# Kernel tuning notes

Measured on AMD Instinct MI355X. Metric: run time of the kernel, lower is better.

The kernel has to match this reference:

```python
import jax, jax.numpy as jnp
import numpy as np

B, S, D, H, E, P, TOP_K = 8, 4096, 512, 2048, 8, 16, 2


def setup_inputs() -> dict:
    key = jax.random.key(0)
    ks = jax.random.split(key, 7)
    x = jax.random.normal(ks[0], (B, S, D), dtype=jnp.float32)
    pattern_ids = jax.random.randint(ks[1], (B,), 0, P)
    # router params (init per module: std 0.01 content, std 0.1 pattern bias)
    Wr = 0.01 * jax.random.normal(ks[2], (D, E), dtype=jnp.float32)
    Wp = 0.1 * jax.random.normal(ks[3], (P, E), dtype=jnp.float32)
    # per-expert SwiGLU FFN weights (stacked): w1, w3: [E,D,H], w2: [E,H,D]
    W1 = jax.random.normal(ks[4], (E, D, H), dtype=jnp.float32) / np.float32(np.sqrt(D))
    W2 = jax.random.normal(ks[5], (E, H, D), dtype=jnp.float32) / np.float32(np.sqrt(H))
    W3 = jax.random.normal(ks[6], (E, D, H), dtype=jnp.float32) / np.float32(np.sqrt(D))
    return {"x": x, "pattern_ids": pattern_ids, "Wr": Wr, "Wp": Wp, "W1": W1, "W2": W2, "W3": W3}


def reference(x, pattern_ids, Wr, Wp, W1, W2, W3):
    num_experts = W1.shape[0]
    num_patterns = Wp.shape[0]
    # ---- pattern-aware router ----
    # content logits + per-batch pattern bias broadcast over seq
    logits = jnp.einsum('bsd,de->bse', x, Wr) + Wp[pattern_ids][:, None, :]  # [B,S,E]
    top_w, top_i = jax.lax.top_k(logits, TOP_K)           # [B,S,K]
    gates = jax.nn.softmax(top_w, axis=-1)                # softmax over the top-k logits
    # ---- expert dispatch / combine (loop over small fixed expert count) ----
    y = jnp.zeros_like(x)
    for e in range(num_experts):
        # combined gate weight for expert e per token (0 if not selected)
        w_e = jnp.sum(gates * (top_i == e), axis=-1)      # [B,S]
        h = jnp.einsum('bsd,dh->bsh', x, W1[e]) * jax.nn.silu(jnp.einsum('bsd,dh->bsh', x, W3[e]))
        y = y + w_e[..., None] * jnp.einsum('bsh,hd->bsd', h, W2[e])
    # ---- auxiliary losses ----
    probs = jax.nn.softmax(logits, axis=-1)
    router_z_loss = jnp.mean(jnp.square(logits)) * 0.001
    balance_loss = jnp.mean(jnp.square(probs.mean(axis=(0, 1)) - 1.0 / num_experts))
    Pn = jax.nn.softmax(Wp, axis=-1)
    sim = Pn @ Pn.T
    specialization_loss = jnp.mean(sim * (1.0 - jnp.eye(num_patterns, dtype=sim.dtype))) * 0.1
    return (y, router_z_loss, balance_loss, specialization_loss)
```

## Files before the change

### kernel.cpp

```cpp
#include <hip/hip_runtime.h>
#include <hip/hip_bf16.h>
#include <math.h>


#define B_ 8
#define S_ 4096
#define D_ 512
#define H_ 2048
#define E_ 8
#define P_ 16
#define NTOK (B_ * S_)
#define NPAIR (NTOK * 2)

typedef __bf16 bf16;
typedef __bf16 bf16x8 __attribute__((ext_vector_type(8)));
typedef float f32x4 __attribute__((ext_vector_type(4)));

#define OFF_GATES 256
#define OFF_LIST (OFF_GATES + NPAIR * 4)
#define OFF_XBF (OFF_LIST + E_ * NTOK * 4)
#define OFF_W13T (OFF_XBF + (size_t)NTOK * D_ * 2)
#define OFF_W2T (OFF_W13T + (size_t)E_ * 2 * H_ * D_ * 2)
#define OFF_HBUF (OFF_W2T + (size_t)E_ * D_ * H_ * 2)
#define WS_NEEDED (OFF_HBUF + (size_t)NTOK * H_ * 2)

__device__ __forceinline__ void gl16(const bf16* g, bf16* l) {
  __builtin_amdgcn_global_load_lds((const __attribute__((address_space(1))) unsigned int*)g,
                                   (__attribute__((address_space(3))) unsigned int*)l, 16, 0, 0);
}

__global__ __launch_bounds__(256) void router_kernel(
    const float* __restrict__ x, const int* __restrict__ pids,
    const float* __restrict__ Wr, const float* __restrict__ Wp,
    bf16* __restrict__ xbf, float* __restrict__ gates, int* __restrict__ lists,
    int* __restrict__ counts, float* __restrict__ probSum, float* __restrict__ zSum) {
  __shared__ float xs[32 * 516];
  __shared__ float wr_s[E_ * 516];
  __shared__ float wp_s[E_];
  __shared__ float probAcc[E_];
  __shared__ float zAcc;
  __shared__ int lcnt[E_], lbase[E_];
  __shared__ float lg_s[32][E_ + 1];

  const int tid = threadIdx.x;
  const int tok0 = blockIdx.x * 32;

#pragma unroll
  for (int rep = 0; rep < (D_ * E_) / 256; ++rep) {
    int flat = rep * 256 + tid;
    wr_s[(flat & 7) * 516 + (flat >> 3)] = Wr[flat];
  }
  if (tid < E_) {
    wp_s[tid] = Wp[pids[tok0 >> 12] * E_ + tid];
    probAcc[tid] = 0.f;
    lcnt[tid] = 0;
  }
  if (tid == 0) zAcc = 0.f;

  const float4* x4 = (const float4*)(x + (size_t)tok0 * D_);
#pragma unroll
  for (int rep = 0; rep < 16; ++rep) {
    int idx = rep * 256 + tid;
    float4 v = x4[idx];
    int t = idx >> 7;
    int d = (idx & 127) * 4;
    *(float4*)(xs + t * 516 + d) = v;
    union { unsigned short u[4]; uint2 qq; } pk;
    pk.u[0] = __builtin_bit_cast(unsigned short, (bf16)v.x);
    pk.u[1] = __builtin_bit_cast(unsigned short, (bf16)v.y);
    pk.u[2] = __builtin_bit_cast(unsigned short, (bf16)v.z);
    pk.u[3] = __builtin_bit_cast(unsigned short, (bf16)v.w);
    *(uint2*)(xbf + (size_t)tok0 * D_ + (size_t)idx * 4) = pk.qq;
  }
  __syncthreads();

  const int t = tid >> 3, e = tid & 7;
  const int lane = tid & 63;
  {
    float a0 = 0.f, a1 = 0.f, a2 = 0.f, a3 = 0.f;
    const float* xr = xs + t * 516;
    const float* wr = wr_s + e * 516;
#pragma unroll 8
    for (int d = 0; d < D_; d += 4) {
      float4 xv = *(const float4*)(xr + d);
      float4 wv = *(const float4*)(wr + d);
      a0 += xv.x * wv.x;
      a1 += xv.y * wv.y;
      a2 += xv.z * wv.z;
      a3 += xv.w * wv.w;
    }
    lg_s[t][e] = (a0 + a1) + (a2 + a3) + wp_s[e];
  }
  __syncthreads();

  float v[E_];
#pragma unroll
  for (int k = 0; k < E_; ++k) v[k] = lg_s[t][k];
  const float lg = v[e];
  float m = v[0];
#pragma unroll
  for (int k = 1; k < E_; ++k) m = fmaxf(m, v[k]);
  float s = 0.f;
#pragma unroll
  for (int k = 0; k < E_; ++k) s += expf(v[k] - m);
  float prob = expf(lg - m) / s;
  float z = lg * lg;
  int i1 = 0;
  float v1 = v[0];
#pragma unroll
  for (int k = 1; k < E_; ++k)
    if (v[k] > v1) { v1 = v[k]; i1 = k; }
  int i2 = -1;
  float v2 = -1e30f;
#pragma unroll
  for (int k = 0; k < E_; ++k)
    if (k != i1 && v[k] > v2) { v2 = v[k]; i2 = k; }

  float p = prob;
  p += __shfl_xor(p, 8);
  p += __shfl_xor(p, 16);
  p += __shfl_xor(p, 32);
  float zz = z;
#pragma unroll
  for (int off = 1; off < 64; off <<= 1) zz += __shfl_xor(zz, off);
  if (lane < 8) atomicAdd(&probAcc[e], p);
  if (lane == 0) atomicAdd(&zAcc, zz);

  int r = (e == i1) ? 0 : ((e == i2) ? 1 : -1);
  int pos = -1;
  if (r >= 0) {
    float ex = expf(v2 - v1);
    float g = (r == 0) ? 1.f / (1.f + ex) : ex / (1.f + ex);
    gates[(tok0 + t) * 2 + r] = g;
    pos = atomicAdd(&lcnt[e], 1);
  }
  __syncthreads();
  if (tid < E_) lbase[tid] = atomicAdd(&counts[tid], lcnt[tid]);
  __syncthreads();
  if (r >= 0) lists[e * NTOK + lbase[e] + pos] = (tok0 + t) * 2 + r;
  if (tid < E_) atomicAdd(&probSum[tid], probAcc[tid]);
  else if (tid == 8) atomicAdd(zSum, zAcc);
}

__global__ __launch_bounds__(256) void transpose_convert(const float* __restrict__ in,
                                                         bf16* __restrict__ out, int R, int C,
                                                         size_t out_estride, int mode) {
  const int e = blockIdx.z;
  const int r0 = blockIdx.y * 64, c0 = blockIdx.x * 64;
  in += (size_t)e * R * C;
  out += (size_t)e * out_estride;
  __shared__ unsigned int lt[64 * 33];

  const int tid = threadIdx.x;
  const int m = tid & 15, qq = tid >> 4;
#pragma unroll
  for (int rep = 0; rep < 2; ++rep) {
    int rp = qq + rep * 16;
    const float4 a = *(const float4*)(in + (size_t)(r0 + rp * 2) * C + c0 + m * 4);
    const float4 b = *(const float4*)(in + (size_t)(r0 + rp * 2 + 1) * C + c0 + m * 4);
#pragma unroll
    for (int j = 0; j < 4; ++j) {
      unsigned short lo = __builtin_bit_cast(unsigned short, (bf16)((&a.x)[j]));
      unsigned short hi = __builtin_bit_cast(unsigned short, (bf16)((&b.x)[j]));
      lt[(m * 4 + j) * 33 + rp] = (unsigned int)lo | ((unsigned int)hi << 16);
    }
  }
  __syncthreads();
  const int c = tid >> 2, dw0 = (tid & 3) * 8;
  unsigned int vv[8];
#pragma unroll
  for (int j = 0; j < 8; ++j) vv[j] = lt[c * 33 + dw0 + j];
  int orow = c0 + c;
  if (mode >= 0) orow = ((orow >> 4) << 5) | (orow & 15) | mode;
  uint4* dst = (uint4*)(out + (size_t)orow * R + r0 + dw0 * 2);
  dst[0] = make_uint4(vv[0], vv[1], vv[2], vv[3]);
  dst[1] = make_uint4(vv[4], vv[5], vv[6], vv[7]);
}

__global__ __launch_bounds__(256, 2) void gemm1_kernel(
    const bf16* __restrict__ xbf, const bf16* __restrict__ W13T,
    const int* __restrict__ counts, const int* __restrict__ lists,
    const float* __restrict__ gates, bf16* __restrict__ hbuf, int e) {
  const int count = counts[e];
  const int m0 = blockIdx.y * 128;
  if (m0 >= count) return;
  const int n0 = blockIdx.x * 128;
  const int* list_e = lists + e * NTOK;
  const bf16* Be = W13T + (size_t)e * (2 * H_) * D_;

  __shared__ bf16 sA[4 * 128 * 32];
  __shared__ bf16 sB[4 * 128 * 32];
  __shared__ int stok[128];
  __shared__ float sgate[128];

  const int tid = threadIdx.x;
  if (tid < 128) {
    int rg = m0 + tid;
    int pr = (rg < count) ? list_e[rg] : 0;
    stok[tid] = pr >> 1;
    sgate[tid] = (rg < count) ? gates[pr] : 0.f;
  }
  __syncthreads();

  const int wave = tid >> 6, lane = tid & 63;
  const int rsub = lane >> 2, kq = lane & 3;
  const int scol = (kq ^ ((lane >> 3) & 3)) * 8;
  const int rA0 = wave * 16 + rsub, rA1 = 64 + wave * 16 + rsub;
  const bf16* aP0 = xbf + (size_t)stok[rA0] * D_ + scol;
  const bf16* aP1 = xbf + (size_t)stok[rA1] * D_ + scol;
  const bf16* bP0 = Be + (size_t)(n0 + rA0) * D_ + scol;
  const bf16* bP1 = Be + (size_t)(n0 + rA1) * D_ + scol;

  const int wm = wave >> 1, wn = wave & 1;
  const int lm = lane & 15, q = lane >> 4;
  const int rq = (q ^ ((lm >> 1) & 3)) * 8;
  const bf16* aRd = sA + (wm * 64 + lm) * 32 + rq;
  const bf16* bRd = sB + (wn * 64 + lm) * 32 + rq;

  f32x4 acc[4][4] = {};

  auto STAGE = [&](int t, int bi) {
    const int ko = t * 32;
    bf16* ba = sA + bi * 4096;
    bf16* bb = sB + bi * 4096;
    gl16(aP0 + ko, ba + wave * 512);
    gl16(aP1 + ko, ba + (wave + 4) * 512);
    gl16(bP0 + ko, bb + wave * 512);
    gl16(bP1 + ko, bb + (wave + 4) * 512);
  };
  auto COMP = [&](int bi) {
    const bf16* aR = aRd + bi * 4096;
    const bf16* bR = bRd + bi * 4096;
    bf16x8 af[4], bf_[4];
#pragma unroll
    for (int i = 0; i < 4; ++i) {
      af[i] = *(const bf16x8*)(aR + i * 512);
      bf_[i] = *(const bf16x8*)(bR + i * 512);
    }
#pragma unroll
    for (int mt = 0; mt < 4; ++mt)
#pragma unroll
      for (int nt = 0; nt < 4; ++nt)
        acc[mt][nt] =
            __builtin_amdgcn_mfma_f32_16x16x32_bf16(af[mt], bf_[nt], acc[mt][nt], 0, 0, 0);
  };

  STAGE(0, 0);
  STAGE(1, 1);
  for (int t = 0; t < D_ / 32 - 2; ++t) {
    STAGE(t + 2, (t + 2) & 3);
    asm volatile("s_waitcnt vmcnt(8) lgkmcnt(0)" ::: "memory");
    __builtin_amdgcn_s_barrier();
    COMP(t & 3);
  }
  asm volatile("s_waitcnt vmcnt(4) lgkmcnt(0)" ::: "memory");
  __builtin_amdgcn_s_barrier();
  COMP((D_ / 32 - 2) & 3);
  asm volatile("s_waitcnt vmcnt(0) lgkmcnt(0)" ::: "memory");
  __builtin_amdgcn_s_barrier();
  COMP((D_ / 32 - 1) & 3);

  const int hb = (n0 >> 1) + wn * 32;
#pragma unroll
  for (int mt = 0; mt < 4; ++mt) {
#pragma unroll
    for (int u = 0; u < 2; ++u) {
#pragma unroll
      for (int r = 0; r < 4; ++r) {
        int lrow = wm * 64 + mt * 16 + q * 4 + r;
        int grow = m0 + lrow;
        if (grow < count) {
          float v1 = acc[mt][2 * u][r];
          float v3 = acc[mt][2 * u + 1][r];
          float g = v1 * (v3 / (1.f + __expf(-v3))) * sgate[lrow];
          hbuf[(size_t)grow * H_ + hb + u * 16 + lm] = (bf16)g;
        }
      }
    }
  }
}

__global__ __launch_bounds__(256, 2) void gemm2_kernel(const bf16* __restrict__ hbuf,
                                                       const bf16* __restrict__ W2T,
                                                       const int* __restrict__ counts,
                                                       const int* __restrict__ lists,
                                                       float* __restrict__ y, int e) {
  const int count = counts[e];
  const int m0 = blockIdx.y * 128;
  if (m0 >= count) return;
  const int n0 = blockIdx.x * 128;
  const int kb = blockIdx.z * (H_ / 2);
  const bf16* W2e = W2T + (size_t)e * D_ * H_;
  const int* list_e = lists + e * NTOK;

  __shared__ bf16 sA[4 * 128 * 32];
  __shared__ bf16 sB[4 * 128 * 32];
  __shared__ int stok[128];

  const int tid = threadIdx.x;
  if (tid < 128) {
    int rg = m0 + tid;
    stok[tid] = (rg < count) ? (list_e[rg] >> 1) : 0;
  }
  __syncthreads();

  const int wave = tid >> 6, lane = tid & 63;
  const int rsub = lane >> 2, kq = lane & 3;
  const int scol = (kq ^ ((lane >> 3) & 3)) * 8;
  const int rA0 = wave * 16 + rsub, rA1 = 64 + wave * 16 + rsub;
  const bf16* aP0 = hbuf + (size_t)(m0 + rA0) * H_ + kb + scol;
  const bf16* aP1 = hbuf + (size_t)(m0 + rA1) * H_ + kb + scol;
  const bf16* bP0 = W2e + (size_t)(n0 + rA0) * H_ + kb + scol;
  const bf16* bP1 = W2e + (size_t)(n0 + rA1) * H_ + kb + scol;

  const int wm = wave >> 1, wn = wave & 1;
  const int lm = lane & 15, q = lane >> 4;
  const int rq = (q ^ ((lm >> 1) & 3)) * 8;
  const bf16* aRd = sA + (wm * 64 + lm) * 32 + rq;
  const bf16* bRd = sB + (wn * 64 + lm) * 32 + rq;

  f32x4 acc[4][4] = {};

  auto STAGE = [&](int t, int bi) {
    const int ko = t * 32;
    bf16* ba = sA + bi * 4096;
    bf16* bb = sB + bi * 4096;
    gl16(aP0 + ko, ba + wave * 512);
    gl16(aP1 + ko, ba + (wave + 4) * 512);
    gl16(bP0 + ko, bb + wave * 512);
    gl16(bP1 + ko, bb + (wave + 4) * 512);
  };
  auto COMP = [&](int bi) {
    const bf16* aR = aRd + bi * 4096;
    const bf16* bR = bRd + bi * 4096;
    bf16x8 af[4], bf_[4];
#pragma unroll
    for (int i = 0; i < 4; ++i) {
      af[i] = *(const bf16x8*)(aR + i * 512);
      bf_[i] = *(const bf16x8*)(bR + i * 512);
    }
#pragma unroll
    for (int mt = 0; mt < 4; ++mt)
#pragma unroll
      for (int nt = 0; nt < 4; ++nt)
        acc[mt][nt] =
            __builtin_amdgcn_mfma_f32_16x16x32_bf16(af[mt], bf_[nt], acc[mt][nt], 0, 0, 0);
  };

  const int NT = (H_ / 2) / 32;
  STAGE(0, 0);
  STAGE(1, 1);
  for (int t = 0; t < NT - 2; ++t) {
    STAGE(t + 2, (t + 2) & 3);
    asm volatile("s_waitcnt vmcnt(8) lgkmcnt(0)" ::: "memory");
    __builtin_amdgcn_s_barrier();
    COMP(t & 3);
  }
  asm volatile("s_waitcnt vmcnt(4) lgkmcnt(0)" ::: "memory");
  __builtin_amdgcn_s_barrier();
  COMP((NT - 2) & 3);
  asm volatile("s_waitcnt vmcnt(0) lgkmcnt(0)" ::: "memory");
  __builtin_amdgcn_s_barrier();
  COMP((NT - 1) & 3);

#pragma unroll
  for (int mt = 0; mt < 4; ++mt) {
#pragma unroll
    for (int nt = 0; nt < 4; ++nt) {
#pragma unroll
      for (int r = 0; r < 4; ++r) {
        int lrow = wm * 64 + mt * 16 + q * 4 + r;
        int grow = m0 + lrow;
        if (grow < count) {
          atomicAdd(&y[(size_t)stok[lrow] * D_ + n0 + wn * 64 + nt * 16 + lm], acc[mt][nt][r]);
        }
      }
    }
  }
}

__global__ __launch_bounds__(256) void finalize_kernel(const float* __restrict__ Wp,
                                                       const float* __restrict__ probSum,
                                                       const float* __restrict__ zSum,
                                                       float* __restrict__ out) {
  __shared__ float pn[P_][E_];
  __shared__ float simAcc;
  const int tid = threadIdx.x;
  if (tid == 0) simAcc = 0.f;
  if (tid < P_) {
    float v[E_], m = -1e30f, s = 0.f;
#pragma unroll
    for (int e = 0; e < E_; ++e) {
      v[e] = Wp[tid * E_ + e];
      m = fmaxf(m, v[e]);
    }
#pragma unroll
    for (int e = 0; e < E_; ++e) {
      float ex = expf(v[e] - m);
      pn[tid][e] = ex;
      s += ex;
    }
#pragma unroll
    for (int e = 0; e < E_; ++e) pn[tid][e] /= s;
  }
  __syncthreads();
  {
    int i = tid >> 4, j = tid & 15;
    if (i != j) {
      float d = 0.f;
#pragma unroll
      for (int e = 0; e < E_; ++e) d += pn[i][e] * pn[j][e];
      atomicAdd(&simAcc, d);
    }
  }
  __syncthreads();
  if (tid == 0) {
    out[0] = zSum[0] / (float)(NTOK * E_) * 0.001f;
    float bl = 0.f;
#pragma unroll
    for (int e = 0; e < E_; ++e) {
      float pm = probSum[e] / (float)NTOK - 1.f / (float)E_;
      bl += pm * pm;
    }
    out[1] = bl / (float)E_;
    out[2] = simAcc / (float)(P_ * P_) * 0.1f;
  }
}

extern "C" void kernel_launch(void* const* d_in, const int* in_sizes, int n_in, void* d_out,
                              int out_size, void* d_ws, size_t ws_size, hipStream_t stream) {
  const float* x = (const float*)d_in[0];
  const int* pids = (const int*)d_in[1];
  const float* Wr = (const float*)d_in[2];
  const float* Wp = (const float*)d_in[3];
  const float* W1 = (const float*)d_in[4];
  const float* W2 = (const float*)d_in[5];
  const float* W3 = (const float*)d_in[6];
  float* y = (float*)d_out;

  if (ws_size < WS_NEEDED) return;

  char* ws = (char*)d_ws;
  int* counts = (int*)ws;
  float* probSum = (float*)(ws + 32);
  float* zSum = (float*)(ws + 64);
  float* gates = (float*)(ws + OFF_GATES);
  int* lists = (int*)(ws + OFF_LIST);
  bf16* xbf = (bf16*)(ws + OFF_XBF);
  bf16* W13T = (bf16*)(ws + OFF_W13T);
  bf16* W2T = (bf16*)(ws + OFF_W2T);
  bf16* hbuf = (bf16*)(ws + OFF_HBUF);

  hipMemsetAsync(ws, 0, 256, stream);
  hipMemsetAsync(d_out, 0, (size_t)NTOK * D_ * 4, stream);

  router_kernel<<<dim3(NTOK / 32), 256, 0, stream>>>(x, pids, Wr, Wp, xbf, gates, lists, counts,
                                                     probSum, zSum);
  transpose_convert<<<dim3(H_ / 64, D_ / 64, E_), 256, 0, stream>>>(W1, W13T, D_, H_,
                                                                    (size_t)2 * H_ * D_, 0);
  transpose_convert<<<dim3(H_ / 64, D_ / 64, E_), 256, 0, stream>>>(W3, W13T, D_, H_,
                                                                    (size_t)2 * H_ * D_, 16);
  transpose_convert<<<dim3(D_ / 64, H_ / 64, E_), 256, 0, stream>>>(W2, W2T, H_, D_,
                                                                    (size_t)H_ * D_, -1);

  for (int e = 0; e < E_; ++e) {
    gemm1_kernel<<<dim3((2 * H_) / 128, NTOK / 128), 256, 0, stream>>>(xbf, W13T, counts, lists,
                                                                       gates, hbuf, e);
    gemm2_kernel<<<dim3(D_ / 128, NTOK / 128, 2), 256, 0, stream>>>(hbuf, W2T, counts, lists, y,
                                                                    e);
  }
  finalize_kernel<<<1, 256, 0, stream>>>(Wp, probSum, zSum, y + (size_t)NTOK * D_);
}
```

Before: 1.111 ms.

## Load A operand directly into registers, bypassing LDS in expert GEMMs

Both expert GEMM kernels stop staging the activation (A) tile through shared memory. Each wave instead loads its MFMA A fragments directly from global memory into double-buffered registers, while B stays in the LDS pipeline. This removes A's LDS writes and reads and halves LDS usage. In exchange, A is fetched twice, once per N-wave, through the cache, and load latency depends on register prefetch depth.

```diff
diff --git a/kernel.cpp b/kernel.cpp
--- a/kernel.cpp
+++ b/kernel.cpp
@@ -28,6 +28,17 @@
   __builtin_amdgcn_global_load_lds((const __attribute__((address_space(1))) unsigned int*)g,
                                    (__attribute__((address_space(3))) unsigned int*)l, 16, 0, 0);
 }
+
+#define WAITV(n)                                                      \
+  do {                                                                \
+    asm volatile("s_waitcnt vmcnt(" #n ") lgkmcnt(0)" ::: "memory");  \
+    __builtin_amdgcn_sched_barrier(0);                                \
+  } while (0)
+#define BARR()                                                        \
+  do {                                                                \
+    __builtin_amdgcn_s_barrier();                                     \
+    __builtin_amdgcn_sched_barrier(0);                                \
+  } while (0)
 
 __global__ __launch_bounds__(256) void router_kernel(
     const float* __restrict__ x, const int* __restrict__ pids,
@@ -188,7 +199,6 @@
   const int* list_e = lists + e * NTOK;
   const bf16* Be = W13T + (size_t)e * (2 * H_) * D_;
 
-  __shared__ bf16 sA[4 * 128 * 32];
   __shared__ bf16 sB[4 * 128 * 32];
   __shared__ int stok[128];
   __shared__ float sgate[128];
@@ -206,37 +216,35 @@
   const int rsub = lane >> 2, kq = lane & 3;
   const int scol = (kq ^ ((lane >> 3) & 3)) * 8;
   const int rA0 = wave * 16 + rsub, rA1 = 64 + wave * 16 + rsub;
-  const bf16* aP0 = xbf + (size_t)stok[rA0] * D_ + scol;
-  const bf16* aP1 = xbf + (size_t)stok[rA1] * D_ + scol;
   const bf16* bP0 = Be + (size_t)(n0 + rA0) * D_ + scol;
   const bf16* bP1 = Be + (size_t)(n0 + rA1) * D_ + scol;
 
   const int wm = wave >> 1, wn = wave & 1;
   const int lm = lane & 15, q = lane >> 4;
   const int rq = (q ^ ((lm >> 1) & 3)) * 8;
-  const bf16* aRd = sA + (wm * 64 + lm) * 32 + rq;
   const bf16* bRd = sB + (wn * 64 + lm) * 32 + rq;
 
+  const bf16* aPtr[4];
+#pragma unroll
+  for (int mt = 0; mt < 4; ++mt)
+    aPtr[mt] = xbf + (size_t)stok[wm * 64 + mt * 16 + lm] * D_ + q * 8;
+
   f32x4 acc[4][4] = {};
 
   auto STAGE = [&](int t, int bi) {
-    const int ko = t * 32;
-    bf16* ba = sA + bi * 4096;
     bf16* bb = sB + bi * 4096;
-    gl16(aP0 + ko, ba + wave * 512);
-    gl16(aP1 + ko, ba + (wave + 4) * 512);
-    gl16(bP0 + ko, bb + wave * 512);
-    gl16(bP1 + ko, bb + (wave + 4) * 512);
-  };
-  auto COMP = [&](int bi) {
-    const bf16* aR = aRd + bi * 4096;
+    gl16(bP0 + t * 32, bb + wave * 512);
+    gl16(bP1 + t * 32, bb + (wave + 4) * 512);
+  };
+  auto LOADA = [&](bf16x8 (&dst)[4], int t) {
+#pragma unroll
+    for (int mt = 0; mt < 4; ++mt) dst[mt] = *(const bf16x8*)(aPtr[mt] + t * 32);
+  };
+  auto COMP = [&](int bi, const bf16x8 (&af)[4]) {
     const bf16* bR = bRd + bi * 4096;
-    bf16x8 af[4], bf_[4];
-#pragma unroll
-    for (int i = 0; i < 4; ++i) {
-      af[i] = *(const bf16x8*)(aR + i * 512);
-      bf_[i] = *(const bf16x8*)(bR + i * 512);
-    }
+    bf16x8 bf_[4];
+#pragma unroll
+    for (int i = 0; i < 4; ++i) bf_[i] = *(const bf16x8*)(bR + i * 512);
 #pragma unroll
     for (int mt = 0; mt < 4; ++mt)
 #pragma unroll
@@ -245,20 +253,31 @@
             __builtin_amdgcn_mfma_f32_16x16x32_bf16(af[mt], bf_[nt], acc[mt][nt], 0, 0, 0);
   };
 
+  const int NT = D_ / 32;
+  bf16x8 aE[4], aO[4];
   STAGE(0, 0);
   STAGE(1, 1);
-  for (int t = 0; t < D_ / 32 - 2; ++t) {
+  LOADA(aE, 0);
+  LOADA(aO, 1);
+  for (int tt = 0; tt < (NT - 2) / 2; ++tt) {
+    const int t = 2 * tt;
     STAGE(t + 2, (t + 2) & 3);
-    asm volatile("s_waitcnt vmcnt(8) lgkmcnt(0)" ::: "memory");
-    __builtin_amdgcn_s_barrier();
-    COMP(t & 3);
-  }
-  asm volatile("s_waitcnt vmcnt(4) lgkmcnt(0)" ::: "memory");
-  __builtin_amdgcn_s_barrier();
-  COMP((D_ / 32 - 2) & 3);
-  asm volatile("s_waitcnt vmcnt(0) lgkmcnt(0)" ::: "memory");
-  __builtin_amdgcn_s_barrier();
-  COMP((D_ / 32 - 1) & 3);
+    WAITV(6);
+    BARR();
+    COMP(t & 3, aE);
+    LOADA(aE, t + 2);
+    STAGE(t + 3, (t + 3) & 3);
+    WAITV(6);
+    BARR();
+    COMP((t + 1) & 3, aO);
+    LOADA(aO, t + 3);
+  }
+  WAITV(4);
+  BARR();
+  COMP((NT - 2) & 3, aE);
+  WAITV(0);
+  BARR();
+  COMP((NT - 1) & 3, aO);
 
   const int hb = (n0 >> 1) + wn * 32;
 #pragma unroll
@@ -293,7 +312,6 @@
   const bf16* W2e = W2T + (size_t)e * D_ * H_;
   const int* list_e = lists + e * NTOK;
 
-  __shared__ bf16 sA[4 * 128 * 32];
   __shared__ bf16 sB[4 * 128 * 32];
   __shared__ int stok[128];
 
@@ -308,37 +326,35 @@
   const int rsub = lane >> 2, kq = lane & 3;
   const int scol = (kq ^ ((lane >> 3) & 3)) * 8;
   const int rA0 = wave * 16 + rsub, rA1 = 64 + wave * 16 + rsub;
-  const bf16* aP0 = hbuf + (size_t)(m0 + rA0) * H_ + kb + scol;
-  const bf16* aP1 = hbuf + (size_t)(m0 + rA1) * H_ + kb + scol;
   const bf16* bP0 = W2e + (size_t)(n0 + rA0) * H_ + kb + scol;
   const bf16* bP1 = W2e + (size_t)(n0 + rA1) * H_ + kb + scol;
 
   const int wm = wave >> 1, wn = wave & 1;
   const int lm = lane & 15, q = lane >> 4;
   const int rq = (q ^ ((lm >> 1) & 3)) * 8;
-  const bf16* aRd = sA + (wm * 64 + lm) * 32 + rq;
   const bf16* bRd = sB + (wn * 64 + lm) * 32 + rq;
 
+  const bf16* aPtr[4];
+#pragma unroll
+  for (int mt = 0; mt < 4; ++mt)
+    aPtr[mt] = hbuf + (size_t)(m0 + wm * 64 + mt * 16 + lm) * H_ + kb + q * 8;
+
   f32x4 acc[4][4] = {};
 
   auto STAGE = [&](int t, int bi) {
-    const int ko = t * 32;
-    bf16* ba = sA + bi * 4096;
     bf16* bb = sB + bi * 4096;
-    gl16(aP0 + ko, ba + wave * 512);
-    gl16(aP1 + ko, ba + (wave + 4) * 512);
-    gl16(bP0 + ko, bb + wave * 512);
-    gl16(bP1 + ko, bb + (wave + 4) * 512);
-  };
-  auto COMP = [&](int bi) {
-    const bf16* aR = aRd + bi * 4096;
+    gl16(bP0 + t * 32, bb + wave * 512);
+    gl16(bP1 + t * 32, bb + (wave + 4) * 512);
+  };
+  auto LOADA = [&](bf16x8 (&dst)[4], int t) {
+#pragma unroll
+    for (int mt = 0; mt < 4; ++mt) dst[mt] = *(const bf16x8*)(aPtr[mt] + t * 32);
+  };
+  auto COMP = [&](int bi, const bf16x8 (&af)[4]) {
     const bf16* bR = bRd + bi * 4096;
-    bf16x8 af[4], bf_[4];
-#pragma unroll
-    for (int i = 0; i < 4; ++i) {
-      af[i] = *(const bf16x8*)(aR + i * 512);
-      bf_[i] = *(const bf16x8*)(bR + i * 512);
-    }
+    bf16x8 bf_[4];
+#pragma unroll
+    for (int i = 0; i < 4; ++i) bf_[i] = *(const bf16x8*)(bR + i * 512);
 #pragma unroll
     for (int mt = 0; mt < 4; ++mt)
 #pragma unroll
@@ -348,20 +364,30 @@
   };
 
   const int NT = (H_ / 2) / 32;
+  bf16x8 aE[4], aO[4];
   STAGE(0, 0);
   STAGE(1, 1);
-  for (int t = 0; t < NT - 2; ++t) {
+  LOADA(aE, 0);
+  LOADA(aO, 1);
+  for (int tt = 0; tt < (NT - 2) / 2; ++tt) {
+    const int t = 2 * tt;
     STAGE(t + 2, (t + 2) & 3);
-    asm volatile("s_waitcnt vmcnt(8) lgkmcnt(0)" ::: "memory");
-    __builtin_amdgcn_s_barrier();
-    COMP(t & 3);
-  }
-  asm volatile("s_waitcnt vmcnt(4) lgkmcnt(0)" ::: "memory");
-  __builtin_amdgcn_s_barrier();
-  COMP((NT - 2) & 3);
-  asm volatile("s_waitcnt vmcnt(0) lgkmcnt(0)" ::: "memory");
-  __builtin_amdgcn_s_barrier();
-  COMP((NT - 1) & 3);
+    WAITV(6);
+    BARR();
+    COMP(t & 3, aE);
+    LOADA(aE, t + 2);
+    STAGE(t + 3, (t + 3) & 3);
+    WAITV(6);
+    BARR();
+    COMP((t + 1) & 3, aO);
+    LOADA(aO, t + 3);
+  }
+  WAITV(4);
+  BARR();
+  COMP((NT - 2) & 3, aE);
+  WAITV(0);
+  BARR();
+  COMP((NT - 1) & 3, aO);
 
 #pragma unroll
   for (int mt = 0; mt < 4; ++mt) {
```

New measurement: 1.453 ms. +30.7%, slower.

## Fuse per-expert GEMM launches into grouped grids with 3-stage LDS pipeline

Applied to the files above, without the earlier changes.

When the workspace is large enough, the per-expert loop of GEMM launches is replaced by one grouped launch per GEMM stage, with the expert index taken from blockIdx.z. Each expert's hidden rows are written at a prefix-sum offset of the expert counts, so the hidden buffer holds all routed pairs. This removes launch overhead and the partly idle tail waves of each small per-expert grid. The LDS ring buffer also shrinks from 4 to 3 stages with the wait and barrier moved before each stage load, which cuts shared memory per block. The down-projection split-K grows from 2 to 4, which adds parallelism but doubles the atomic adds into y.

```diff
diff --git a/kernel.cpp b/kernel.cpp
--- a/kernel.cpp
+++ b/kernel.cpp
@@ -23,6 +23,7 @@
 #define OFF_W2T (OFF_W13T + (size_t)E_ * 2 * H_ * D_ * 2)
 #define OFF_HBUF (OFF_W2T + (size_t)E_ * D_ * H_ * 2)
 #define WS_NEEDED (OFF_HBUF + (size_t)NTOK * H_ * 2)
+#define WS_FUSED (OFF_HBUF + (size_t)NPAIR * H_ * 2)
 
 __device__ __forceinline__ void gl16(const bf16* g, bf16* l) {
   __builtin_amdgcn_global_load_lds((const __attribute__((address_space(1))) unsigned int*)g,
@@ -180,16 +181,22 @@
 __global__ __launch_bounds__(256, 2) void gemm1_kernel(
     const bf16* __restrict__ xbf, const bf16* __restrict__ W13T,
     const int* __restrict__ counts, const int* __restrict__ lists,
-    const float* __restrict__ gates, bf16* __restrict__ hbuf, int e) {
+    const float* __restrict__ gates, bf16* __restrict__ hbuf, int e_param, int fuse) {
+  const int e = fuse ? (int)blockIdx.z : e_param;
   const int count = counts[e];
   const int m0 = blockIdx.y * 128;
   if (m0 >= count) return;
+  int hbase = 0;
+  if (fuse) {
+#pragma unroll
+    for (int j = 0; j < E_; ++j) hbase += (j < e) ? counts[j] : 0;
+  }
   const int n0 = blockIdx.x * 128;
   const int* list_e = lists + e * NTOK;
   const bf16* Be = W13T + (size_t)e * (2 * H_) * D_;
 
-  __shared__ bf16 sA[4 * 128 * 32];
-  __shared__ bf16 sB[4 * 128 * 32];
+  __shared__ bf16 sA[3 * 128 * 32];
+  __shared__ bf16 sB[3 * 128 * 32];
   __shared__ int stok[128];
   __shared__ float sgate[128];
 
@@ -245,20 +252,23 @@
             __builtin_amdgcn_mfma_f32_16x16x32_bf16(af[mt], bf_[nt], acc[mt][nt], 0, 0, 0);
   };
 
+  const int NT = D_ / 32;
   STAGE(0, 0);
   STAGE(1, 1);
-  for (int t = 0; t < D_ / 32 - 2; ++t) {
-    STAGE(t + 2, (t + 2) & 3);
-    asm volatile("s_waitcnt vmcnt(8) lgkmcnt(0)" ::: "memory");
+  int bi2 = 2;
+  for (int t = 0; t < NT - 2; ++t) {
+    asm volatile("s_waitcnt vmcnt(4) lgkmcnt(0)" ::: "memory");
     __builtin_amdgcn_s_barrier();
-    COMP(t & 3);
+    STAGE(t + 2, bi2);
+    COMP(t == 0 ? 0 : (bi2 == 2 ? 0 : bi2 + 1));
+    bi2 = (bi2 == 2) ? 0 : bi2 + 1;
   }
   asm volatile("s_waitcnt vmcnt(4) lgkmcnt(0)" ::: "memory");
   __builtin_amdgcn_s_barrier();
-  COMP((D_ / 32 - 2) & 3);
+  COMP((NT - 2) % 3);
   asm volatile("s_waitcnt vmcnt(0) lgkmcnt(0)" ::: "memory");
   __builtin_amdgcn_s_barrier();
-  COMP((D_ / 32 - 1) & 3);
+  COMP((NT - 1) % 3);
 
   const int hb = (n0 >> 1) + wn * 32;
 #pragma unroll
@@ -273,7 +283,7 @@
           float v1 = acc[mt][2 * u][r];
           float v3 = acc[mt][2 * u + 1][r];
           float g = v1 * (v3 / (1.f + __expf(-v3))) * sgate[lrow];
-          hbuf[(size_t)grow * H_ + hb + u * 16 + lm] = (bf16)g;
+          hbuf[(size_t)(hbase + grow) * H_ + hb + u * 16 + lm] = (bf16)g;
         }
       }
     }
@@ -284,17 +294,26 @@
                                                        const bf16* __restrict__ W2T,
                                                        const int* __restrict__ counts,
                                                        const int* __restrict__ lists,
-                                                       float* __restrict__ y, int e) {
+                                                       float* __restrict__ y, int e_param,
+                                                       int fuse) {
+  const int zz = (int)blockIdx.z;
+  const int e = fuse ? (zz >> 2) : e_param;
+  const int kc = fuse ? (zz & 3) : zz;
   const int count = counts[e];
   const int m0 = blockIdx.y * 128;
   if (m0 >= count) return;
+  int hbase = 0;
+  if (fuse) {
+#pragma unroll
+    for (int j = 0; j < E_; ++j) hbase += (j < e) ? counts[j] : 0;
+  }
   const int n0 = blockIdx.x * 128;
-  const int kb = blockIdx.z * (H_ / 2);
+  const int kb = kc * (H_ / 4);
   const bf16* W2e = W2T + (size_t)e * D_ * H_;
   const int* list_e = lists + e * NTOK;
 
-  __shared__ bf16 sA[4 * 128 * 32];
-  __shared__ bf16 sB[4 * 128 * 32];
+  __shared__ bf16 sA[3 * 128 * 32];
+  __shared__ bf16 sB[3 * 128 * 32];
   __shared__ int stok[128];
 
   const int tid = threadIdx.x;
@@ -308,8 +327,8 @@
   const int rsub = lane >> 2, kq = lane & 3;
   const int scol = (kq ^ ((lane >> 3) & 3)) * 8;
   const int rA0 = wave * 16 + rsub, rA1 = 64 + wave * 16 + rsub;
-  const bf16* aP0 = hbuf + (size_t)(m0 + rA0) * H_ + kb + scol;
-  const bf16* aP1 = hbuf + (size_t)(m0 + rA1) * H_ + kb + scol;
+  const bf16* aP0 = hbuf + (size_t)(hbase + m0 + rA0) * H_ + kb + scol;
+  const bf16* aP1 = hbuf + (size_t)(hbase + m0 + rA1) * H_ + kb + scol;
   const bf16* bP0 = W2e + (size_t)(n0 + rA0) * H_ + kb + scol;
   const bf16* bP1 = W2e + (size_t)(n0 + rA1) * H_ + kb + scol;
 
@@ -347,21 +366,23 @@
             __builtin_amdgcn_mfma_f32_16x16x32_bf16(af[mt], bf_[nt], acc[mt][nt], 0, 0, 0);
   };
 
-  const int NT = (H_ / 2) / 32;
+  const int NT = (H_ / 4) / 32;
   STAGE(0, 0);
   STAGE(1, 1);
+  int bi2 = 2;
   for (int t = 0; t < NT - 2; ++t) {
-    STAGE(t + 2, (t + 2) & 3);
-    asm volatile("s_waitcnt vmcnt(8) lgkmcnt(0)" ::: "memory");
+    asm volatile("s_waitcnt vmcnt(4) lgkmcnt(0)" ::: "memory");
     __builtin_amdgcn_s_barrier();
-    COMP(t & 3);
+    STAGE(t + 2, bi2);
+    COMP(bi2 == 2 ? 0 : bi2 + 1);
+    bi2 = (bi2 == 2) ? 0 : bi2 + 1;
   }
   asm volatile("s_waitcnt vmcnt(4) lgkmcnt(0)" ::: "memory");
   __builtin_amdgcn_s_barrier();
-  COMP((NT - 2) & 3);
+  COMP((NT - 2) % 3);
   asm volatile("s_waitcnt vmcnt(0) lgkmcnt(0)" ::: "memory");
   __builtin_amdgcn_s_barrier();
-  COMP((NT - 1) & 3);
+  COMP((NT - 1) % 3);
 
 #pragma unroll
   for (int mt = 0; mt < 4; ++mt) {
@@ -439,6 +460,7 @@
   float* y = (float*)d_out;
 
   if (ws_size < WS_NEEDED) return;
+  const int fuse = (ws_size >= WS_FUSED) ? 1 : 0;
 
   char* ws = (char*)d_ws;
   int* counts = (int*)ws;
@@ -463,11 +485,18 @@
   transpose_convert<<<dim3(D_ / 64, H_ / 64, E_), 256, 0, stream>>>(W2, W2T, H_, D_,
                                                                     (size_t)H_ * D_, -1);
 
-  for (int e = 0; e < E_; ++e) {
-    gemm1_kernel<<<dim3((2 * H_) / 128, NTOK / 128), 256, 0, stream>>>(xbf, W13T, counts, lists,
-                                                                       gates, hbuf, e);
-    gemm2_kernel<<<dim3(D_ / 128, NTOK / 128, 2), 256, 0, stream>>>(hbuf, W2T, counts, lists, y,
-                                                                    e);
+  if (fuse) {
+    gemm1_kernel<<<dim3((2 * H_) / 128, NTOK / 128, E_), 256, 0, stream>>>(
+        xbf, W13T, counts, lists, gates, hbuf, 0, 1);
+    gemm2_kernel<<<dim3(D_ / 128, NTOK / 128, 4 * E_), 256, 0, stream>>>(hbuf, W2T, counts,
+                                                                         lists, y, 0, 1);
+  } else {
+    for (int e = 0; e < E_; ++e) {
+      gemm1_kernel<<<dim3((2 * H_) / 128, NTOK / 128), 256, 0, stream>>>(xbf, W13T, counts,
+                                                                         lists, gates, hbuf, e, 0);
+      gemm2_kernel<<<dim3(D_ / 128, NTOK / 128, 4), 256, 0, stream>>>(hbuf, W2T, counts, lists,
+                                                                      y, e, 0);
+    }
   }
   finalize_kernel<<<1, 256, 0, stream>>>(Wp, probSum, zSum, y + (size_t)NTOK * D_);
 }
```

New measurement: 1.229 ms. +10.6%, slower.
